# Kernel optimization log

Hardware: AMD Instinct MI355X
Metric: run time of the kernel (lower is better)

## Reference

```python
import jax, jax.numpy as jnp
import numpy as np

EPS = 1e-08
K_N = 10
K_E = 10
F_DIM = 512
SCALE = F_DIM ** -0.5
N_NODES = 16384
N_EDGES = 2048


def layernorm(x, w, b):
    mu = x.mean(axis=-1, keepdims=True)
    var = x.var(axis=-1, keepdims=True)
    return (x - mu) * jax.lax.rsqrt(var + 1e-5) * w + b


def mask_attn(attn, k):
    # topk along last dim, scatter boolean mask, elementwise masking
    _, idx = jax.lax.top_k(attn, k)
    rows = jnp.arange(attn.shape[0])[:, None]
    mask = jnp.zeros(attn.shape, dtype=bool).at[rows, idx].set(True)
    return attn * mask


def setup_inputs() -> dict:
    key = jax.random.key(0)
    ks = jax.random.split(key, 12)
    d, h = F_DIM, 512  # hidden = max(f_dim, 128)
    w = 0.02  # weight init scale to keep softmax unsaturated
    return {
        'inputs': jax.random.normal(ks[0], (N_NODES, d), jnp.float32),
        'noise': jax.random.normal(ks[1], (N_EDGES, d), jnp.float32),
        'edges_mu': jax.random.normal(ks[2], (1, d), jnp.float32),
        'edges_logsigma': jnp.zeros((1, d), jnp.float32),
        'Wq': jax.random.normal(ks[3], (d, d), jnp.float32) * w,
        'bq': jnp.zeros((d,), jnp.float32),
        'Wk': jax.random.normal(ks[4], (d, d), jnp.float32) * w,
        'bk': jnp.zeros((d,), jnp.float32),
        'Wv': jax.random.normal(ks[5], (d, d), jnp.float32) * w,
        'bv': jnp.zeros((d,), jnp.float32),
        'W1': jax.random.normal(ks[6], (2 * d, h), jnp.float32) * w,
        'b1': jnp.zeros((h,), jnp.float32),
        'W2': jax.random.normal(ks[7], (h, d), jnp.float32) * w,
        'b2': jnp.zeros((d,), jnp.float32),
        'ln_in_w': jnp.ones((d,), jnp.float32),
        'ln_in_b': jnp.zeros((d,), jnp.float32),
        'ln_e_w': jnp.ones((d,), jnp.float32),
        'ln_e_b': jnp.zeros((d,), jnp.float32),
    }


def reference(inputs, noise, edges_mu, edges_logsigma, Wq, bq, Wk, bk, Wv, bv,
              W1, b1, W2, b2, ln_in_w, ln_in_b, ln_e_w, ln_e_b):
    relu = jax.nn.relu
    # slot init: mu + sigma * noise  -> [n_s, d]
    edges = edges_mu + jnp.exp(edges_logsigma) * noise
    x = layernorm(inputs, ln_in_w, ln_in_b)          # [n, d]
    k = relu(x @ Wk + bk)                            # [n, d]
    v = relu(x @ Wv + bv)                            # [n, d]
    # single iteration (iters=1)
    e = layernorm(edges, ln_e_w, ln_e_b)             # [n_s, d]
    q = relu(e @ Wq + bq)                            # [n_s, d]
    dots = (q @ k.T) * SCALE                         # [n_s, n]
    attn = jax.nn.softmax(dots, axis=1) + EPS
    attn = attn / attn.sum(axis=1, keepdims=True)
    attn = mask_attn(attn, K_N)
    updates = attn @ v                               # [n_s, d]
    e = jnp.concatenate([e, updates], axis=1)        # [n_s, 2d]
    e = relu(e @ W1 + b1) @ W2 + b2                  # mlp -> [n_s, d]
    q2 = x @ Wq + bq                                 # note: no activation here
    k2 = relu(e @ Wk + bk)                           # [n_s, d]
    dots2 = (q2 @ k2.T) * SCALE                      # [n, n_s]
    attn_v = jax.nn.softmax(dots2, axis=1)
    H = mask_attn(attn_v, K_E)
    return e, H, dots2
```

## Files before the change

### kernel.cpp

```cpp
#include <hip/hip_runtime.h>
#include <stdint.h>


#define NN 16384
#define NE 2048
#define TOPK 10

static const float SCALE_F = 0.04419417382415922f;
#define EPS_F 1e-8f

using bf16x8  = __attribute__((ext_vector_type(8))) __bf16;
using floatx4 = __attribute__((ext_vector_type(4))) float;

__device__ __forceinline__ unsigned f_as_u(float f) {
  union { float f; unsigned u; } v; v.f = f; return v.u;
}
__device__ __forceinline__ float u_as_f(unsigned u) {
  union { unsigned u; float f; } v; v.u = u; return v.f;
}

__device__ __forceinline__ unsigned short f2bf(float f) {
  unsigned u = f_as_u(f);
  unsigned r = u + 0x7fffu + ((u >> 16) & 1u);
  return (unsigned short)(r >> 16);
}
__device__ __forceinline__ float bf2f(unsigned short h) {
  return u_as_f(((unsigned)h) << 16);
}

__device__ __forceinline__ unsigned fkey(float f) {
  unsigned u = f_as_u(f);
  return (u & 0x80000000u) ? ~u : (u | 0x80000000u);
}
__device__ __forceinline__ float funkey(unsigned k) {
  unsigned u = (k & 0x80000000u) ? (k ^ 0x80000000u) : ~k;
  return u_as_f(u);
}
__device__ __forceinline__ unsigned long long packkc(float v, int col) {
  return ((unsigned long long)fkey(v) << 32) | (unsigned)(~(unsigned)col);
}
__device__ __forceinline__ int unpack_col(unsigned long long w) {
  return (int)(~(unsigned)(w & 0xFFFFFFFFull));
}
__device__ __forceinline__ float unpack_val(unsigned long long w) {
  return funkey((unsigned)(w >> 32));
}
__device__ __forceinline__ unsigned long long shfl_xor_u64(unsigned long long x, int m) {
  unsigned lo = (unsigned)x, hi = (unsigned)(x >> 32);
  lo = __shfl_xor(lo, m, 64);
  hi = __shfl_xor(hi, m, 64);
  return ((unsigned long long)hi << 32) | lo;
}

__global__ void transpose_cast_kernel(const float* __restrict__ src,
                                      unsigned short* __restrict__ dhi,
                                      unsigned short* __restrict__ dlo,
                                      int K, int N) {
  __shared__ float tile[32][33];
  int n0 = blockIdx.x * 32, k0 = blockIdx.y * 32;
  int tx = threadIdx.x, ty = threadIdx.y;
  for (int r = ty; r < 32; r += 8)
    tile[r][tx] = src[(size_t)(k0 + r) * N + n0 + tx];
  __syncthreads();
  for (int r = ty; r < 32; r += 8) {
    float v = tile[tx][r];
    size_t o = (size_t)(n0 + r) * K + k0 + tx;
    unsigned short h = f2bf(v);
    dhi[o] = h;
    if (dlo) dlo[o] = f2bf(v - bf2f(h));
  }
}

__device__ __forceinline__ float block_sum_256(float v, float* sm4) {
#pragma unroll
  for (int off = 32; off; off >>= 1) v += __shfl_down(v, off, 64);
  __syncthreads();
  if ((threadIdx.x & 63) == 0) sm4[threadIdx.x >> 6] = v;
  __syncthreads();
  return (sm4[0] + sm4[1]) + (sm4[2] + sm4[3]);
}

__global__ __launch_bounds__(256) void ln_x_kernel(
    const float* __restrict__ in, const float* __restrict__ w,
    const float* __restrict__ b, unsigned short* __restrict__ out_hi) {
  __shared__ float sm4[4];
  int row = blockIdx.x, tid = threadIdx.x;
  const float* r = in + (size_t)row * 512;
  float x0 = r[tid], x1 = r[tid + 256];
  float mu = block_sum_256(x0 + x1, sm4) * (1.0f / 512.0f);
  float d0 = x0 - mu, d1 = x1 - mu;
  float var = block_sum_256(d0 * d0 + d1 * d1, sm4) * (1.0f / 512.0f);
  float rs = rsqrtf(var + 1e-5f);
  out_hi[(size_t)row * 512 + tid]       = f2bf(d0 * rs * w[tid] + b[tid]);
  out_hi[(size_t)row * 512 + tid + 256] = f2bf(d1 * rs * w[tid + 256] + b[tid + 256]);
}

__global__ __launch_bounds__(256) void ln_e_kernel(
    const float* __restrict__ noise, const float* __restrict__ mu_e,
    const float* __restrict__ ls_e, const float* __restrict__ w,
    const float* __restrict__ b, unsigned short* __restrict__ e1_hi,
    unsigned short* __restrict__ e1_lo) {
  __shared__ float sm4[4];
  int row = blockIdx.x, tid = threadIdx.x;
  const float* r = noise + (size_t)row * 512;
  float x0 = mu_e[tid] + expf(ls_e[tid]) * r[tid];
  float x1 = mu_e[tid + 256] + expf(ls_e[tid + 256]) * r[tid + 256];
  float mu = block_sum_256(x0 + x1, sm4) * (1.0f / 512.0f);
  float d0 = x0 - mu, d1 = x1 - mu;
  float var = block_sum_256(d0 * d0 + d1 * d1, sm4) * (1.0f / 512.0f);
  float rs = rsqrtf(var + 1e-5f);
  float y0 = d0 * rs * w[tid] + b[tid];
  float y1 = d1 * rs * w[tid + 256] + b[tid + 256];
  size_t o = (size_t)row * 1024;
  unsigned short h0 = f2bf(y0), h1 = f2bf(y1);
  e1_hi[o + tid] = h0;             e1_lo[o + tid] = f2bf(y0 - bf2f(h0));
  e1_hi[o + tid + 256] = h1;       e1_lo[o + tid + 256] = f2bf(y1 - bf2f(h1));
}

template <bool RELU, bool HAS_BIAS, bool WF32, bool WBF16>
__global__ __launch_bounds__(256) void gemm128_kernel(
    const unsigned short* __restrict__ A, int lda,
    const unsigned short* __restrict__ B, int K,
    const float* __restrict__ bias, float alpha,
    float* __restrict__ Cf, int ldc,
    unsigned short* __restrict__ Cb, int ldcb) {
  __shared__ __align__(16) unsigned short As[128 * 32];
  __shared__ __align__(16) unsigned short Bs[128 * 32];
  int tid = threadIdx.x;
  int wave = tid >> 6, lane = tid & 63;
  int lrow = lane & 15, quad = lane >> 4;
  size_t bm = (size_t)blockIdx.x * 128, bn = (size_t)blockIdx.y * 128;

  int c0 = tid, c1 = tid + 256;
  const unsigned short* pA0 = A + (bm + (c0 >> 2)) * lda + ((c0 & 3) << 3);
  const unsigned short* pA1 = A + (bm + (c1 >> 2)) * lda + ((c1 & 3) << 3);
  const unsigned short* pB0 = B + (bn + (c0 >> 2)) * (size_t)K + ((c0 & 3) << 3);
  const unsigned short* pB1 = B + (bn + (c1 >> 2)) * (size_t)K + ((c1 & 3) << 3);

  floatx4 zero4 = {0.f, 0.f, 0.f, 0.f};
  floatx4 acc[2][8];
#pragma unroll
  for (int i = 0; i < 2; ++i)
#pragma unroll
    for (int t = 0; t < 8; ++t) acc[i][t] = zero4;

  for (int k0 = 0; k0 < K; k0 += 32) {
    uint4 a0 = *(const uint4*)(pA0 + k0);
    uint4 a1 = *(const uint4*)(pA1 + k0);
    uint4 b0 = *(const uint4*)(pB0 + k0);
    uint4 b1 = *(const uint4*)(pB1 + k0);
    __syncthreads();
    *(uint4*)&As[c0 * 8] = a0;
    *(uint4*)&As[c1 * 8] = a1;
    *(uint4*)&Bs[c0 * 8] = b0;
    *(uint4*)&Bs[c1 * 8] = b1;
    __syncthreads();
    bf16x8 af0 = *(const bf16x8*)&As[(wave * 32 + lrow) * 32 + quad * 8];
    bf16x8 af1 = *(const bf16x8*)&As[(wave * 32 + 16 + lrow) * 32 + quad * 8];
#pragma unroll
    for (int t = 0; t < 8; ++t) {
      bf16x8 bfr = *(const bf16x8*)&Bs[(t * 16 + lrow) * 32 + quad * 8];
      acc[0][t] = __builtin_amdgcn_mfma_f32_16x16x32_bf16(af0, bfr, acc[0][t], 0, 0, 0);
      acc[1][t] = __builtin_amdgcn_mfma_f32_16x16x32_bf16(af1, bfr, acc[1][t], 0, 0, 0);
    }
  }
#pragma unroll
  for (int i = 0; i < 2; ++i) {
    size_t row0 = bm + wave * 32 + i * 16 + quad * 4;
#pragma unroll
    for (int t = 0; t < 8; ++t) {
      int col = (int)bn + t * 16 + lrow;
      float bv = HAS_BIAS ? bias[col] : 0.0f;
#pragma unroll
      for (int r = 0; r < 4; ++r) {
        float v = acc[i][t][r] * alpha + bv;
        if (RELU) v = fmaxf(v, 0.0f);
        if (WF32) Cf[(row0 + r) * (size_t)ldc + col] = v;
        if (WBF16) Cb[(row0 + r) * (size_t)ldcb + col] = f2bf(v);
      }
    }
  }
}

template <bool SPLIT, bool RELU, bool HAS_BIAS, bool WF32, bool WHI, bool WLO>
__global__ __launch_bounds__(256) void gemm64_kernel(
    const unsigned short* __restrict__ Ahi, const unsigned short* __restrict__ Alo, int lda,
    const unsigned short* __restrict__ Bhi, const unsigned short* __restrict__ Blo, int K,
    const float* __restrict__ bias, float alpha,
    float* __restrict__ Cf, int ldc,
    unsigned short* __restrict__ Chi, unsigned short* __restrict__ Clo, int ldcb) {
  __shared__ __align__(16) unsigned short AsH[64 * 32];
  __shared__ __align__(16) unsigned short BsH[64 * 32];
  __shared__ __align__(16) unsigned short AsL[64 * 32];
  __shared__ __align__(16) unsigned short BsL[64 * 32];
  int tid = threadIdx.x, wave = tid >> 6, lane = tid & 63;
  int lrow = lane & 15, quad = lane >> 4;
  size_t bm = (size_t)blockIdx.x * 64, bn = (size_t)blockIdx.y * 64;
  int row = tid >> 2, off = (tid & 3) << 3;
  size_t aoff = (bm + row) * (size_t)lda + off;
  size_t boff = (bn + row) * (size_t)K + off;

  floatx4 zero4 = {0.f, 0.f, 0.f, 0.f};
  floatx4 acc[4];
#pragma unroll
  for (int t = 0; t < 4; ++t) acc[t] = zero4;

  for (int k0 = 0; k0 < K; k0 += 32) {
    uint4 ah = *(const uint4*)(Ahi + aoff + k0);
    uint4 bh = *(const uint4*)(Bhi + boff + k0);
    uint4 al, bl;
    if (SPLIT) {
      al = *(const uint4*)(Alo + aoff + k0);
      bl = *(const uint4*)(Blo + boff + k0);
    }
    __syncthreads();
    *(uint4*)&AsH[tid * 8] = ah;
    *(uint4*)&BsH[tid * 8] = bh;
    if (SPLIT) {
      *(uint4*)&AsL[tid * 8] = al;
      *(uint4*)&BsL[tid * 8] = bl;
    }
    __syncthreads();
    int ai = (wave * 16 + lrow) * 32 + quad * 8;
    bf16x8 aH = *(const bf16x8*)&AsH[ai];
    bf16x8 aL;
    if (SPLIT) aL = *(const bf16x8*)&AsL[ai];
#pragma unroll
    for (int t = 0; t < 4; ++t) {
      int bi = (t * 16 + lrow) * 32 + quad * 8;
      bf16x8 bH = *(const bf16x8*)&BsH[bi];
      acc[t] = __builtin_amdgcn_mfma_f32_16x16x32_bf16(aH, bH, acc[t], 0, 0, 0);
      if (SPLIT) {
        bf16x8 bL = *(const bf16x8*)&BsL[bi];
        acc[t] = __builtin_amdgcn_mfma_f32_16x16x32_bf16(aH, bL, acc[t], 0, 0, 0);
        acc[t] = __builtin_amdgcn_mfma_f32_16x16x32_bf16(aL, bH, acc[t], 0, 0, 0);
      }
    }
  }
  size_t row0 = bm + wave * 16 + quad * 4;
#pragma unroll
  for (int t = 0; t < 4; ++t) {
    int col = (int)bn + t * 16 + lrow;
    float bv = HAS_BIAS ? bias[col] : 0.0f;
#pragma unroll
    for (int r = 0; r < 4; ++r) {
      float v = acc[t][r] * alpha + bv;
      if (RELU) v = fmaxf(v, 0.0f);
      if (WF32) Cf[(row0 + r) * (size_t)ldc + col] = v;
      if (WHI) {
        unsigned short h = f2bf(v);
        Chi[(row0 + r) * (size_t)ldcb + col] = h;
        if (WLO) Clo[(row0 + r) * (size_t)ldcb + col] = f2bf(v - bf2f(h));
      }
    }
  }
}

#define INSERT4(lv, li, v, col)                                   \
  do {                                                            \
    if ((v) > lv[3]) {                                            \
      float cv_ = (v); int ci_ = (col);                           \
      _Pragma("unroll")                                           \
      for (int j_ = 0; j_ < 4; ++j_) {                            \
        bool sw_ = (cv_ > lv[j_]);                                \
        float tv_ = sw_ ? lv[j_] : cv_;                           \
        int ti_ = sw_ ? li[j_] : ci_;                              \
        lv[j_] = sw_ ? cv_ : lv[j_];                              \
        li[j_] = sw_ ? ci_ : li[j_];                              \
        cv_ = tv_; ci_ = ti_;                                     \
      }                                                           \
    }                                                             \
  } while (0)

__global__ __launch_bounds__(256) void attn1_kernel(
    const float* __restrict__ dots,
    const unsigned short* __restrict__ vhi,
    unsigned short* __restrict__ e1_hi, unsigned short* __restrict__ e1_lo) {
  __shared__ float sm_m[4], sm_s[4];
  __shared__ unsigned long long wbest[4];
  __shared__ unsigned long long wkey_s[TOPK];

  int tid = threadIdx.x, wave = tid >> 6, lane = tid & 63;
  int rowi = blockIdx.x;
  const float4* r4 = (const float4*)(dots + (size_t)rowi * NN);

  float lv[4]; int li[4];
#pragma unroll
  for (int j = 0; j < 4; ++j) { lv[j] = -INFINITY; li[j] = 0x7fffffff; }
  unsigned long long selmask = 0ull;
  int taken = 0;

  float m_loc = -INFINITY, s_loc = 0.0f;
  for (int i = 0; i < 16; ++i) {
    float4 q = r4[tid + (i << 8)];
#pragma unroll
    for (int c = 0; c < 4; ++c) {
      float v = (&q.x)[c];
      int col = ((tid + (i << 8)) << 2) + c;
      if (v > m_loc) {
        s_loc = s_loc * __expf(m_loc - v) + 1.0f;
        m_loc = v;
      } else {
        s_loc += __expf(v - m_loc);
      }
      INSERT4(lv, li, v, col);
    }
  }
#pragma unroll
  for (int sft = 32; sft; sft >>= 1) {
    float om = __shfl_xor(m_loc, sft, 64);
    float os = __shfl_xor(s_loc, sft, 64);
    float M = fmaxf(m_loc, om);
    s_loc = s_loc * __expf(m_loc - M) + os * __expf(om - M);
    m_loc = M;
  }
  if (lane == 0) { sm_m[wave] = m_loc; sm_s[wave] = s_loc; }
  __syncthreads();
  float M = fmaxf(fmaxf(sm_m[0], sm_m[1]), fmaxf(sm_m[2], sm_m[3]));
  float Z = sm_s[0] * __expf(sm_m[0] - M) + sm_s[1] * __expf(sm_m[1] - M) +
            sm_s[2] * __expf(sm_m[2] - M) + sm_s[3] * __expf(sm_m[3] - M);

  for (int rnd = 0; rnd < TOPK; ++rnd) {
    unsigned long long key;
    if (taken < 4) {
      key = packkc(lv[0], li[0]);
    } else {
      key = 0ull;
      for (int i = 0; i < 16; ++i) {
        float4 q = r4[tid + (i << 8)];
#pragma unroll
        for (int c = 0; c < 4; ++c) {
          int sl = i * 4 + c;
          if (!((selmask >> sl) & 1ull)) {
            int col = ((tid + (i << 8)) << 2) + c;
            unsigned long long kk = packkc((&q.x)[c], col);
            if (kk > key) key = kk;
          }
        }
      }
    }
#pragma unroll
    for (int sft = 32; sft; sft >>= 1) {
      unsigned long long ok = shfl_xor_u64(key, sft);
      if (ok > key) key = ok;
    }
    if (lane == 0) wbest[wave] = key;
    __syncthreads();
    unsigned long long w = wbest[0];
    if (wbest[1] > w) w = wbest[1];
    if (wbest[2] > w) w = wbest[2];
    if (wbest[3] > w) w = wbest[3];
    if (tid == 0) wkey_s[rnd] = w;
    int wcol = unpack_col(w);
    if (((wcol >> 2) & 255) == tid) {
      int sl = ((wcol >> 10) << 2) | (wcol & 3);
      selmask |= (1ull << sl);
      if (taken < 4) {
#pragma unroll
        for (int j = 0; j < 3; ++j) { lv[j] = lv[j + 1]; li[j] = li[j + 1]; }
      }
      ++taken;
    }
    __syncthreads();
  }

  const float inv_den = 1.0f / (1.0f + (float)NN * EPS_F);
  float invZ = 1.0f / Z;
  float u0 = 0.f, u1 = 0.f;
#pragma unroll
  for (int j = 0; j < TOPK; ++j) {
    unsigned long long w = wkey_s[j];
    int col = unpack_col(w);
    float val = unpack_val(w);
    float a = (__expf(val - M) * invZ + EPS_F) * inv_den;
    const unsigned short* vr = vhi + (size_t)col * 512;
    u0 += a * bf2f(vr[tid]);
    u1 += a * bf2f(vr[tid + 256]);
  }
  size_t o = (size_t)rowi * 1024 + 512;
  unsigned short h0 = f2bf(u0), h1 = f2bf(u1);
  e1_hi[o + tid] = h0;             e1_lo[o + tid] = f2bf(u0 - bf2f(h0));
  e1_hi[o + tid + 256] = h1;       e1_lo[o + tid + 256] = f2bf(u1 - bf2f(h1));
}

__global__ __launch_bounds__(256) void attn2_kernel(const float* __restrict__ dots2,
                                                    float* __restrict__ Hout) {
  int tid = threadIdx.x, wave = tid >> 6, lane = tid & 63;
  int rowi = blockIdx.x * 4 + wave;
  const float4* r4 = (const float4*)(dots2 + (size_t)rowi * NE);

  float d[32];
  float m = -INFINITY;
#pragma unroll
  for (int i = 0; i < 8; ++i) {
    float4 q = r4[lane + (i << 6)];
#pragma unroll
    for (int c = 0; c < 4; ++c) {
      d[i * 4 + c] = (&q.x)[c];
      m = fmaxf(m, d[i * 4 + c]);
    }
  }
#pragma unroll
  for (int sft = 32; sft; sft >>= 1) m = fmaxf(m, __shfl_xor(m, sft, 64));

  float s = 0.f;
#pragma unroll
  for (int j = 0; j < 32; ++j) { d[j] = __expf(d[j] - m); s += d[j]; }
#pragma unroll
  for (int sft = 32; sft; sft >>= 1) s += __shfl_xor(s, sft, 64);
  float invZ = 1.0f / s;

  float lv[4]; int li[4];
#pragma unroll
  for (int j = 0; j < 4; ++j) { lv[j] = -INFINITY; li[j] = 0x7fffffff; }
#pragma unroll
  for (int i = 0; i < 8; ++i) {
#pragma unroll
    for (int c = 0; c < 4; ++c) {
      int col = ((lane + (i << 6)) << 2) + c;
      INSERT4(lv, li, d[i * 4 + c], col);
    }
  }

  unsigned selmask = 0;
  int taken = 0;
  for (int rnd = 0; rnd < TOPK; ++rnd) {
    unsigned long long key;
    if (taken < 4) {
      key = packkc(lv[0], li[0]);
    } else {
      key = 0ull;
#pragma unroll
      for (int j = 0; j < 32; ++j) {
        if (!((selmask >> j) & 1u)) {
          int col = ((lane + ((j >> 2) << 6)) << 2) + (j & 3);
          unsigned long long kk = packkc(d[j], col);
          if (kk > key) key = kk;
        }
      }
    }
#pragma unroll
    for (int sft = 32; sft; sft >>= 1) {
      unsigned long long ok = shfl_xor_u64(key, sft);
      if (ok > key) key = ok;
    }
    int wcol = unpack_col(key);
    if (((wcol >> 2) & 63) == lane) {
      int sl = ((wcol >> 8) << 2) | (wcol & 3);
      selmask |= (1u << sl);
      if (taken < 4) {
#pragma unroll
        for (int j = 0; j < 3; ++j) { lv[j] = lv[j + 1]; li[j] = li[j + 1]; }
      }
      ++taken;
    }
  }

  float* hr = Hout + (size_t)rowi * NE;
#pragma unroll
  for (int i = 0; i < 8; ++i) {
    float4 o;
#pragma unroll
    for (int c = 0; c < 4; ++c) {
      int sl = i * 4 + c;
      (&o.x)[c] = ((selmask >> sl) & 1u) ? d[sl] * invZ : 0.0f;
    }
    ((float4*)hr)[lane + (i << 6)] = o;
  }
}

extern "C" void kernel_launch(void* const* d_in, const int* in_sizes, int n_in,
                              void* d_out, int out_size, void* d_ws, size_t ws_size,
                              hipStream_t stream) {
  (void)in_sizes; (void)n_in; (void)out_size; (void)ws_size;
  const float* inputs  = (const float*)d_in[0];
  const float* noise   = (const float*)d_in[1];
  const float* edges_mu = (const float*)d_in[2];
  const float* edges_ls = (const float*)d_in[3];
  const float* Wq = (const float*)d_in[4];
  const float* bq = (const float*)d_in[5];
  const float* Wk = (const float*)d_in[6];
  const float* bk = (const float*)d_in[7];
  const float* Wv = (const float*)d_in[8];
  const float* bv = (const float*)d_in[9];
  const float* W1 = (const float*)d_in[10];
  const float* b1 = (const float*)d_in[11];
  const float* W2 = (const float*)d_in[12];
  const float* b2 = (const float*)d_in[13];
  const float* ln_in_w = (const float*)d_in[14];
  const float* ln_in_b = (const float*)d_in[15];
  const float* ln_e_w = (const float*)d_in[16];
  const float* ln_e_b = (const float*)d_in[17];

  float* out_e  = (float*)d_out;
  float* out_H  = out_e + (size_t)NE * 512;
  float* out_d2 = out_H + (size_t)NN * NE;

  const size_t MB = 1024 * 1024;
  unsigned char* sc = (unsigned char*)out_d2;
  unsigned short* x_hi  = (unsigned short*)(sc);
  unsigned short* k_hi  = (unsigned short*)(sc + 16 * MB);
  unsigned short* v_hi  = (unsigned short*)(sc + 32 * MB);
  unsigned short* WqT   = (unsigned short*)(sc + 48 * MB);
  unsigned short* WkT   = (unsigned short*)(sc + 48 * MB + 512 * 1024);
  unsigned short* WvT   = (unsigned short*)(sc + 48 * MB + 1024 * 1024);
  unsigned short* W1Th  = (unsigned short*)(sc + 48 * MB + 1536 * 1024);
  unsigned short* W1Tl  = (unsigned short*)(sc + 48 * MB + 2560 * 1024);
  unsigned short* W2Th  = (unsigned short*)(sc + 48 * MB + 3584 * 1024);
  unsigned short* W2Tl  = (unsigned short*)(sc + 48 * MB + 4096 * 1024);
  unsigned short* e1_hi = (unsigned short*)(sc + 56 * MB);
  unsigned short* e1_lo = (unsigned short*)(sc + 60 * MB);
  unsigned short* q_hi  = (unsigned short*)(sc + 64 * MB);
  unsigned short* h_hi  = (unsigned short*)(sc + 66 * MB);
  unsigned short* h_lo  = (unsigned short*)(sc + 68 * MB);
  unsigned short* e_hi  = (unsigned short*)(sc + 70 * MB);
  float* dots = out_H;
  unsigned short* q2_hi = (unsigned short*)out_H;
  unsigned short* k2_hi = (unsigned short*)d_ws;

  dim3 tb(256);
  dim3 t32(32, 8);

  transpose_cast_kernel<<<dim3(16, 16), t32, 0, stream>>>(Wq, WqT, nullptr, 512, 512);
  transpose_cast_kernel<<<dim3(16, 16), t32, 0, stream>>>(Wk, WkT, nullptr, 512, 512);
  transpose_cast_kernel<<<dim3(16, 16), t32, 0, stream>>>(Wv, WvT, nullptr, 512, 512);
  transpose_cast_kernel<<<dim3(16, 32), t32, 0, stream>>>(W1, W1Th, W1Tl, 1024, 512);
  transpose_cast_kernel<<<dim3(16, 16), t32, 0, stream>>>(W2, W2Th, W2Tl, 512, 512);

  ln_x_kernel<<<NN, tb, 0, stream>>>(inputs, ln_in_w, ln_in_b, x_hi);
  ln_e_kernel<<<NE, tb, 0, stream>>>(noise, edges_mu, edges_ls, ln_e_w, ln_e_b, e1_hi, e1_lo);

  gemm128_kernel<true, true, false, true><<<dim3(128, 4), tb, 0, stream>>>(
      x_hi, 512, WkT, 512, bk, 1.f, nullptr, 0, k_hi, 512);
  gemm128_kernel<true, true, false, true><<<dim3(128, 4), tb, 0, stream>>>(
      x_hi, 512, WvT, 512, bv, 1.f, nullptr, 0, v_hi, 512);
  gemm64_kernel<false, true, true, false, true, false><<<dim3(32, 8), tb, 0, stream>>>(
      e1_hi, nullptr, 1024, WqT, nullptr, 512, bq, 1.f, nullptr, 0, q_hi, nullptr, 512);
  gemm128_kernel<false, false, true, false><<<dim3(16, 128), tb, 0, stream>>>(
      q_hi, 512, k_hi, 512, nullptr, SCALE_F, dots, NN, nullptr, 0);
  attn1_kernel<<<NE, tb, 0, stream>>>(dots, v_hi, e1_hi, e1_lo);
  gemm64_kernel<true, true, true, false, true, true><<<dim3(32, 8), tb, 0, stream>>>(
      e1_hi, e1_lo, 1024, W1Th, W1Tl, 1024, b1, 1.f, nullptr, 0, h_hi, h_lo, 512);
  gemm64_kernel<true, false, true, true, true, false><<<dim3(32, 8), tb, 0, stream>>>(
      h_hi, h_lo, 512, W2Th, W2Tl, 512, b2, 1.f, out_e, 512, e_hi, nullptr, 512);
  gemm64_kernel<false, true, true, false, true, false><<<dim3(32, 8), tb, 0, stream>>>(
      e_hi, nullptr, 512, WkT, nullptr, 512, bk, 1.f, nullptr, 0, k2_hi, nullptr, 512);
  gemm128_kernel<false, true, false, true><<<dim3(128, 4), tb, 0, stream>>>(
      x_hi, 512, WqT, 512, bq, 1.f, nullptr, 0, q2_hi, 512);
  gemm128_kernel<false, false, true, false><<<dim3(128, 16), tb, 0, stream>>>(
      q2_hi, 512, k2_hi, 512, nullptr, SCALE_F, out_d2, NE, nullptr, 0);
  attn2_kernel<<<NN / 4, tb, 0, stream>>>(out_d2, out_H);
}
```

Before: 614.5 us.

## Fuse K/V/Q2 projections into one GEMM with direct global-to-LDS loads

The three x-projections (k, v, q2) now run as one GEMM against a concatenated transposed weight matrix, and the three weight transposes become one launch. The GEMM inner loop uses global_load_lds to copy tiles straight into shared memory instead of staging them through registers, which removes the register round-trip and the copy instructions. Scratch buffers move from the dots2 output region into the H output region to make room for the layout change. The cost is a second barrier per k-step and the use of a lower-level builtin whose LDS layout must match the per-wave destination mapping.

```diff
diff --git a/kernel.cpp b/kernel.cpp
--- a/kernel.cpp
+++ b/kernel.cpp
@@ -18,7 +18,6 @@
 __device__ __forceinline__ float u_as_f(unsigned u) {
   union { unsigned u; float f; } v; v.u = u; return v.f;
 }
-
 __device__ __forceinline__ unsigned short f2bf(float f) {
   unsigned u = f_as_u(f);
   unsigned r = u + 0x7fffu + ((u >> 16) & 1u);
@@ -26,6 +25,12 @@
 }
 __device__ __forceinline__ float bf2f(unsigned short h) {
   return u_as_f(((unsigned)h) << 16);
+}
+
+__device__ __forceinline__ void glds16(const unsigned short* g, unsigned short* l) {
+  __builtin_amdgcn_global_load_lds(
+      (const __attribute__((address_space(1))) unsigned int*)g,
+      (__attribute__((address_space(3))) unsigned int*)l, 16, 0, 0);
 }
 
 __device__ __forceinline__ unsigned fkey(float f) {
@@ -69,6 +74,22 @@
     dhi[o] = h;
     if (dlo) dlo[o] = f2bf(v - bf2f(h));
   }
+}
+
+__global__ void transpose_cast3_kernel(const float* __restrict__ s0,
+                                       const float* __restrict__ s1,
+                                       const float* __restrict__ s2,
+                                       unsigned short* __restrict__ dhi) {
+  __shared__ float tile[32][33];
+  const float* src = blockIdx.z == 0 ? s0 : (blockIdx.z == 1 ? s1 : s2);
+  unsigned short* d = dhi + (size_t)blockIdx.z * 512 * 512;
+  int n0 = blockIdx.x * 32, k0 = blockIdx.y * 32;
+  int tx = threadIdx.x, ty = threadIdx.y;
+  for (int r = ty; r < 32; r += 8)
+    tile[r][tx] = src[(size_t)(k0 + r) * 512 + n0 + tx];
+  __syncthreads();
+  for (int r = ty; r < 32; r += 8)
+    d[(size_t)(n0 + r) * 512 + k0 + tx] = f2bf(tile[tx][r]);
 }
 
 __device__ __forceinline__ float block_sum_256(float v, float* sm4) {
@@ -117,66 +138,95 @@
   e1_hi[o + tid + 256] = h1;       e1_lo[o + tid + 256] = f2bf(y1 - bf2f(h1));
 }
 
-template <bool RELU, bool HAS_BIAS, bool WF32, bool WBF16>
-__global__ __launch_bounds__(256) void gemm128_kernel(
-    const unsigned short* __restrict__ A, int lda,
-    const unsigned short* __restrict__ B, int K,
-    const float* __restrict__ bias, float alpha,
-    float* __restrict__ Cf, int ldc,
-    unsigned short* __restrict__ Cb, int ldcb) {
-  __shared__ __align__(16) unsigned short As[128 * 32];
-  __shared__ __align__(16) unsigned short Bs[128 * 32];
-  int tid = threadIdx.x;
-  int wave = tid >> 6, lane = tid & 63;
+#define GEMM128_CORE(A_, B_, bm_, bn_, acc_)                                   \
+  __shared__ __align__(16) unsigned short As[128 * 32];                        \
+  __shared__ __align__(16) unsigned short Bs[128 * 32];                        \
+  {                                                                            \
+    const unsigned short* gA0 = (A_) + ((bm_) + (tid >> 2)) * 512 + ((tid & 3) << 3); \
+    const unsigned short* gA1 = gA0 + 64 * 512;                                \
+    const unsigned short* gB0 = (B_) + ((bn_) + (tid >> 2)) * 512 + ((tid & 3) << 3); \
+    const unsigned short* gB1 = gB0 + 64 * 512;                                \
+    unsigned short* dA0 = &As[wave * 512];                                     \
+    unsigned short* dA1 = &As[2048 + wave * 512];                              \
+    unsigned short* dB0 = &Bs[wave * 512];                                     \
+    unsigned short* dB1 = &Bs[2048 + wave * 512];                              \
+    for (int k0 = 0; k0 < 512; k0 += 32) {                                     \
+      glds16(gA0 + k0, dA0);                                                   \
+      glds16(gA1 + k0, dA1);                                                   \
+      glds16(gB0 + k0, dB0);                                                   \
+      glds16(gB1 + k0, dB1);                                                   \
+      __syncthreads();                                                         \
+      bf16x8 af0 = *(const bf16x8*)&As[(wave * 32 + lrow) * 32 + quad * 8];    \
+      bf16x8 af1 = *(const bf16x8*)&As[(wave * 32 + 16 + lrow) * 32 + quad * 8]; \
+      _Pragma("unroll")                                                        \
+      for (int t = 0; t < 8; ++t) {                                            \
+        bf16x8 bfr = *(const bf16x8*)&Bs[(t * 16 + lrow) * 32 + quad * 8];     \
+        acc_[0][t] = __builtin_amdgcn_mfma_f32_16x16x32_bf16(af0, bfr, acc_[0][t], 0, 0, 0); \
+        acc_[1][t] = __builtin_amdgcn_mfma_f32_16x16x32_bf16(af1, bfr, acc_[1][t], 0, 0, 0); \
+      }                                                                        \
+      __syncthreads();                                                         \
+    }                                                                          \
+  }
+
+__global__ __launch_bounds__(256) void gemm128_dots_kernel(
+    const unsigned short* __restrict__ A, const unsigned short* __restrict__ B,
+    float alpha, float* __restrict__ C, int ldc) {
+  int tid = threadIdx.x, wave = tid >> 6, lane = tid & 63;
   int lrow = lane & 15, quad = lane >> 4;
   size_t bm = (size_t)blockIdx.x * 128, bn = (size_t)blockIdx.y * 128;
-
-  int c0 = tid, c1 = tid + 256;
-  const unsigned short* pA0 = A + (bm + (c0 >> 2)) * lda + ((c0 & 3) << 3);
-  const unsigned short* pA1 = A + (bm + (c1 >> 2)) * lda + ((c1 & 3) << 3);
-  const unsigned short* pB0 = B + (bn + (c0 >> 2)) * (size_t)K + ((c0 & 3) << 3);
-  const unsigned short* pB1 = B + (bn + (c1 >> 2)) * (size_t)K + ((c1 & 3) << 3);
-
   floatx4 zero4 = {0.f, 0.f, 0.f, 0.f};
   floatx4 acc[2][8];
 #pragma unroll
   for (int i = 0; i < 2; ++i)
 #pragma unroll
     for (int t = 0; t < 8; ++t) acc[i][t] = zero4;
-
-  for (int k0 = 0; k0 < K; k0 += 32) {
-    uint4 a0 = *(const uint4*)(pA0 + k0);
-    uint4 a1 = *(const uint4*)(pA1 + k0);
-    uint4 b0 = *(const uint4*)(pB0 + k0);
-    uint4 b1 = *(const uint4*)(pB1 + k0);
-    __syncthreads();
-    *(uint4*)&As[c0 * 8] = a0;
-    *(uint4*)&As[c1 * 8] = a1;
-    *(uint4*)&Bs[c0 * 8] = b0;
-    *(uint4*)&Bs[c1 * 8] = b1;
-    __syncthreads();
-    bf16x8 af0 = *(const bf16x8*)&As[(wave * 32 + lrow) * 32 + quad * 8];
-    bf16x8 af1 = *(const bf16x8*)&As[(wave * 32 + 16 + lrow) * 32 + quad * 8];
-#pragma unroll
-    for (int t = 0; t < 8; ++t) {
-      bf16x8 bfr = *(const bf16x8*)&Bs[(t * 16 + lrow) * 32 + quad * 8];
-      acc[0][t] = __builtin_amdgcn_mfma_f32_16x16x32_bf16(af0, bfr, acc[0][t], 0, 0, 0);
-      acc[1][t] = __builtin_amdgcn_mfma_f32_16x16x32_bf16(af1, bfr, acc[1][t], 0, 0, 0);
-    }
-  }
+  GEMM128_CORE(A, B, bm, bn, acc)
 #pragma unroll
   for (int i = 0; i < 2; ++i) {
     size_t row0 = bm + wave * 32 + i * 16 + quad * 4;
 #pragma unroll
     for (int t = 0; t < 8; ++t) {
       int col = (int)bn + t * 16 + lrow;
-      float bv = HAS_BIAS ? bias[col] : 0.0f;
+#pragma unroll
+      for (int r = 0; r < 4; ++r)
+        C[(row0 + r) * (size_t)ldc + col] = acc[i][t][r] * alpha;
+    }
+  }
+}
+
+__global__ __launch_bounds__(256) void gemm128_kvq_kernel(
+    const unsigned short* __restrict__ A, const unsigned short* __restrict__ B,
+    const float* __restrict__ bk, const float* __restrict__ bv,
+    const float* __restrict__ bq,
+    unsigned short* __restrict__ khi, unsigned short* __restrict__ vhi,
+    unsigned short* __restrict__ q2hi) {
+  int tid = threadIdx.x, wave = tid >> 6, lane = tid & 63;
+  int lrow = lane & 15, quad = lane >> 4;
+  size_t bm = (size_t)blockIdx.x * 128, bn = (size_t)blockIdx.y * 128;
+  floatx4 zero4 = {0.f, 0.f, 0.f, 0.f};
+  floatx4 acc[2][8];
+#pragma unroll
+  for (int i = 0; i < 2; ++i)
+#pragma unroll
+    for (int t = 0; t < 8; ++t) acc[i][t] = zero4;
+  GEMM128_CORE(A, B, bm, bn, acc)
+  int mat = (int)(bn >> 9);
+  int colbase = (int)(bn & 511);
+  const float* bias = mat == 0 ? bk : (mat == 1 ? bv : bq);
+  unsigned short* dst = mat == 0 ? khi : (mat == 1 ? vhi : q2hi);
+  bool relu = mat < 2;
+#pragma unroll
+  for (int i = 0; i < 2; ++i) {
+    size_t row0 = bm + wave * 32 + i * 16 + quad * 4;
+#pragma unroll
+    for (int t = 0; t < 8; ++t) {
+      int col = colbase + t * 16 + lrow;
+      float bvv = bias[col];
 #pragma unroll
       for (int r = 0; r < 4; ++r) {
-        float v = acc[i][t][r] * alpha + bv;
-        if (RELU) v = fmaxf(v, 0.0f);
-        if (WF32) Cf[(row0 + r) * (size_t)ldc + col] = v;
-        if (WBF16) Cb[(row0 + r) * (size_t)ldcb + col] = f2bf(v);
+        float v = acc[i][t][r] + bvv;
+        if (relu) v = fmaxf(v, 0.0f);
+        dst[(row0 + r) * 512 + col] = f2bf(v);
       }
     }
   }
@@ -497,47 +547,42 @@
   float* out_d2 = out_H + (size_t)NN * NE;
 
   const size_t MB = 1024 * 1024;
-  unsigned char* sc = (unsigned char*)out_d2;
-  unsigned short* x_hi  = (unsigned short*)(sc);
-  unsigned short* k_hi  = (unsigned short*)(sc + 16 * MB);
-  unsigned short* v_hi  = (unsigned short*)(sc + 32 * MB);
-  unsigned short* WqT   = (unsigned short*)(sc + 48 * MB);
-  unsigned short* WkT   = (unsigned short*)(sc + 48 * MB + 512 * 1024);
-  unsigned short* WvT   = (unsigned short*)(sc + 48 * MB + 1024 * 1024);
-  unsigned short* W1Th  = (unsigned short*)(sc + 48 * MB + 1536 * 1024);
-  unsigned short* W1Tl  = (unsigned short*)(sc + 48 * MB + 2560 * 1024);
-  unsigned short* W2Th  = (unsigned short*)(sc + 48 * MB + 3584 * 1024);
-  unsigned short* W2Tl  = (unsigned short*)(sc + 48 * MB + 4096 * 1024);
-  unsigned short* e1_hi = (unsigned short*)(sc + 56 * MB);
-  unsigned short* e1_lo = (unsigned short*)(sc + 60 * MB);
-  unsigned short* q_hi  = (unsigned short*)(sc + 64 * MB);
-  unsigned short* h_hi  = (unsigned short*)(sc + 66 * MB);
-  unsigned short* h_lo  = (unsigned short*)(sc + 68 * MB);
-  unsigned short* e_hi  = (unsigned short*)(sc + 70 * MB);
-  float* dots = out_H;
-  unsigned short* q2_hi = (unsigned short*)out_H;
+  unsigned char* hb = (unsigned char*)out_H;
+  unsigned short* x_hi  = (unsigned short*)(hb);
+  unsigned short* k_hi  = (unsigned short*)(hb + 16 * MB);
+  unsigned short* v_hi  = (unsigned short*)(hb + 32 * MB);
+  unsigned short* q2_hi = (unsigned short*)(hb + 48 * MB);
+  unsigned short* WcatT = (unsigned short*)(hb + 64 * MB);
+  unsigned short* W1Th  = (unsigned short*)(hb + 66 * MB);
+  unsigned short* W1Tl  = (unsigned short*)(hb + 67 * MB);
+  unsigned short* W2Th  = (unsigned short*)(hb + 68 * MB);
+  unsigned short* W2Tl  = (unsigned short*)(hb + 68 * MB + 512 * 1024);
+  unsigned short* e1_hi = (unsigned short*)(hb + 70 * MB);
+  unsigned short* e1_lo = (unsigned short*)(hb + 74 * MB);
+  unsigned short* q_hi  = (unsigned short*)(hb + 78 * MB);
+  unsigned short* h_hi  = (unsigned short*)(hb + 80 * MB);
+  unsigned short* h_lo  = (unsigned short*)(hb + 82 * MB);
+  unsigned short* e_hi  = (unsigned short*)(hb + 84 * MB);
+  unsigned short* WkT   = WcatT;
+  unsigned short* WqT   = WcatT + (size_t)1024 * 512;
+  float* dots = out_d2;
   unsigned short* k2_hi = (unsigned short*)d_ws;
 
   dim3 tb(256);
   dim3 t32(32, 8);
 
-  transpose_cast_kernel<<<dim3(16, 16), t32, 0, stream>>>(Wq, WqT, nullptr, 512, 512);
-  transpose_cast_kernel<<<dim3(16, 16), t32, 0, stream>>>(Wk, WkT, nullptr, 512, 512);
-  transpose_cast_kernel<<<dim3(16, 16), t32, 0, stream>>>(Wv, WvT, nullptr, 512, 512);
+  transpose_cast3_kernel<<<dim3(16, 16, 3), t32, 0, stream>>>(Wk, Wv, Wq, WcatT);
   transpose_cast_kernel<<<dim3(16, 32), t32, 0, stream>>>(W1, W1Th, W1Tl, 1024, 512);
   transpose_cast_kernel<<<dim3(16, 16), t32, 0, stream>>>(W2, W2Th, W2Tl, 512, 512);
 
   ln_x_kernel<<<NN, tb, 0, stream>>>(inputs, ln_in_w, ln_in_b, x_hi);
   ln_e_kernel<<<NE, tb, 0, stream>>>(noise, edges_mu, edges_ls, ln_e_w, ln_e_b, e1_hi, e1_lo);
 
-  gemm128_kernel<true, true, false, true><<<dim3(128, 4), tb, 0, stream>>>(
-      x_hi, 512, WkT, 512, bk, 1.f, nullptr, 0, k_hi, 512);
-  gemm128_kernel<true, true, false, true><<<dim3(128, 4), tb, 0, stream>>>(
-      x_hi, 512, WvT, 512, bv, 1.f, nullptr, 0, v_hi, 512);
+  gemm128_kvq_kernel<<<dim3(128, 12), tb, 0, stream>>>(
+      x_hi, WcatT, bk, bv, bq, k_hi, v_hi, q2_hi);
   gemm64_kernel<false, true, true, false, true, false><<<dim3(32, 8), tb, 0, stream>>>(
       e1_hi, nullptr, 1024, WqT, nullptr, 512, bq, 1.f, nullptr, 0, q_hi, nullptr, 512);
-  gemm128_kernel<false, false, true, false><<<dim3(16, 128), tb, 0, stream>>>(
-      q_hi, 512, k_hi, 512, nullptr, SCALE_F, dots, NN, nullptr, 0);
+  gemm128_dots_kernel<<<dim3(16, 128), tb, 0, stream>>>(q_hi, k_hi, SCALE_F, dots, NN);
   attn1_kernel<<<NE, tb, 0, stream>>>(dots, v_hi, e1_hi, e1_lo);
   gemm64_kernel<true, true, true, false, true, true><<<dim3(32, 8), tb, 0, stream>>>(
       e1_hi, e1_lo, 1024, W1Th, W1Tl, 1024, b1, 1.f, nullptr, 0, h_hi, h_lo, 512);
@@ -545,9 +590,6 @@
       h_hi, h_lo, 512, W2Th, W2Tl, 512, b2, 1.f, out_e, 512, e_hi, nullptr, 512);
   gemm64_kernel<false, true, true, false, true, false><<<dim3(32, 8), tb, 0, stream>>>(
       e_hi, nullptr, 512, WkT, nullptr, 512, bk, 1.f, nullptr, 0, k2_hi, nullptr, 512);
-  gemm128_kernel<false, true, false, true><<<dim3(128, 4), tb, 0, stream>>>(
-      x_hi, 512, WqT, 512, bq, 1.f, nullptr, 0, q2_hi, 512);
-  gemm128_kernel<false, false, true, false><<<dim3(128, 16), tb, 0, stream>>>(
-      q2_hi, 512, k2_hi, 512, nullptr, SCALE_F, out_d2, NE, nullptr, 0);
+  gemm128_dots_kernel<<<dim3(128, 16), tb, 0, stream>>>(q2_hi, k2_hi, SCALE_F, out_d2, NE);
   attn2_kernel<<<NN / 4, tb, 0, stream>>>(out_d2, out_H);
 }
```

Measured after the change: 572.8 us. 6.8% less time.
